# Kernel tuning notes

Hardware: AMD Instinct MI355X
Metric: run time of the kernel (lower is better)

## Reference

```python
import jax, jax.numpy as jnp
import numpy as np

N_FP = 235336   # n_fingerprint
N_WORD = 7844   # n_word
D = 10          # embed / hidden dim (hard-coded in module)
K = 23          # conv kernel 2*11+1
PAD = 11
N_ATOMS = 4096
L_WORDS = 65536


def setup_inputs() -> dict:
    key = jax.random.key(0)
    ks = jax.random.split(key, 16)
    s = 0.1  # weight init scale
    return {
        "fingerprints": jax.random.randint(ks[0], (N_ATOMS,), 0, N_FP),
        # scale adjacency so x + A@hs stays O(1) over 3 layers
        "adjacency": jax.random.uniform(ks[1], (N_ATOMS, N_ATOMS), dtype=jnp.float32) * (1.0 / N_ATOMS),
        "words": jax.random.randint(ks[2], (L_WORDS,), 0, N_WORD),
        "embed_fp": jax.random.normal(ks[3], (N_FP, D), dtype=jnp.float32) * s,
        "embed_word": jax.random.normal(ks[4], (N_WORD, D), dtype=jnp.float32) * s,
        "W_gnn_w": jax.random.normal(ks[5], (3, D, D), dtype=jnp.float32) * s,
        "W_gnn_b": jax.random.normal(ks[6], (3, D), dtype=jnp.float32) * s,
        "W_cnn_w": jax.random.normal(ks[7], (3, 1, 1, K, K), dtype=jnp.float32) * (s / K),
        "W_cnn_b": jax.random.normal(ks[8], (3,), dtype=jnp.float32) * s,
        "W_att_w": jax.random.normal(ks[9], (D, D), dtype=jnp.float32) * s,
        "W_att_b": jax.random.normal(ks[10], (D,), dtype=jnp.float32) * s,
        "W_out_w": jax.random.normal(ks[11], (3, 2 * D, 2 * D), dtype=jnp.float32) * s,
        "W_out_b": jax.random.normal(ks[12], (3, 2 * D), dtype=jnp.float32) * s,
        "W_int_w": jax.random.normal(ks[13], (2, 2 * D), dtype=jnp.float32) * s,
        "W_int_b": jax.random.normal(ks[14], (2,), dtype=jnp.float32) * s,
    }


def reference(fingerprints, adjacency, words, embed_fp, embed_word,
              W_gnn_w, W_gnn_b, W_cnn_w, W_cnn_b, W_att_w, W_att_b,
              W_out_w, W_out_b, W_int_w, W_int_b):
    # ---- Compound vector with GNN ----
    xs = embed_fp[fingerprints]                       # [N, D]
    for i in range(3):                                # fixed 3 layers
        hs = jax.nn.relu(xs @ W_gnn_w[i].T + W_gnn_b[i])
        xs = xs + adjacency @ hs                      # dense message passing
    compound = jnp.mean(xs, axis=0, keepdims=True)    # [1, D]

    # ---- Protein vector with attention-CNN ----
    ws = embed_word[words]                            # [L, D]
    t = ws[None, None]                                # [1,1,L,D] NCHW
    for i in range(3):
        t = jax.nn.relu(
            jax.lax.conv_general_dilated(t, W_cnn_w[i], (1, 1),
                                          [(PAD, PAD), (PAD, PAD)])
            + W_cnn_b[i])
    xs_p = t[0, 0]                                    # [L, D]

    h = jax.nn.relu(compound @ W_att_w.T + W_att_b)   # [1, D]
    hs_p = jax.nn.relu(xs_p @ W_att_w.T + W_att_b)    # [L, D]
    weights = jnp.tanh(h @ hs_p.T)                    # [1, L]
    ys = weights.T * hs_p                             # [L, D]
    protein = jnp.mean(ys, axis=0, keepdims=True)     # [1, D]

    # ---- Fusion MLP ----
    cat = jnp.concatenate([compound, protein], axis=1)  # [1, 2D]
    for j in range(3):
        cat = jax.nn.relu(cat @ W_out_w[j].T + W_out_b[j])
    return cat @ W_int_w.T + W_int_b                  # [1, 2]
```

## Files before the change

### kernel.cpp

```cpp
#include <hip/hip_runtime.h>
#include <math.h>

#define N_ATOMS 4096
#define L_WORDS 65536
#define DD 10
#define HALO 11

#define CONV_BLOCKS 256
#define CONV_BLOCK 256
#define RPW 8
#define RPB 32
#define QCOLS 1024
#define TOTAL_BLOCKS 768
#define ATT_BLOCKS 64

__global__ __launch_bounds__(128) void gnn_embed(
    const int* __restrict__ fp, const float* __restrict__ embed_fp,
    const float* __restrict__ Wg, const float* __restrict__ bg,
    float* __restrict__ xs, float* __restrict__ hs)
{
    const int n = blockIdx.x * 128 + threadIdx.x;
    float x[DD];
    const float* e = embed_fp + (size_t)fp[n] * DD;
    #pragma unroll
    for (int d = 0; d < DD; ++d) x[d] = e[d];
    #pragma unroll
    for (int d = 0; d < DD; ++d) xs[d * N_ATOMS + n] = x[d];
    #pragma unroll
    for (int d = 0; d < DD; ++d) {
        float v = bg[d];
        #pragma unroll
        for (int k = 0; k < DD; ++k) v += Wg[d * DD + k] * x[k];
        hs[d * N_ATOMS + n] = fmaxf(v, 0.f);
    }
}

__device__ __forceinline__ void conv_stage(
    float* sh, const int tid, const int bx,
    const float* __restrict__ tin, const int* __restrict__ words,
    const float* __restrict__ embed_word, const float* __restrict__ w,
    const float* __restrict__ bptr, float* __restrict__ tout,
    const float* __restrict__ Wa, const float* __restrict__ ba,
    float* __restrict__ hpb)
{
    const int l0 = bx * CONV_BLOCK;
    for (int idx = tid; idx < (CONV_BLOCK + 2 * HALO) * DD; idx += CONV_BLOCK) {
        int rr = idx / DD, d = idx - rr * DD;
        int gr = l0 - HALO + rr;
        float v = 0.f;
        if (gr >= 0 && gr < L_WORDS) {
            if (tin) v = tin[(size_t)gr * DD + d];
            else     v = embed_word[(size_t)words[gr] * DD + d];
        }
        sh[rr * 11 + d] = v;
    }
    __syncthreads();

    const float bias = *bptr;
    float acc[DD];
    #pragma unroll
    for (int d = 0; d < DD; ++d) acc[d] = bias;
    for (int i = 0; i < 23; ++i) {
        float row[DD];
        const float* sr = &sh[(tid + i) * 11];
        #pragma unroll
        for (int c = 0; c < DD; ++c) row[c] = sr[c];
        #pragma unroll
        for (int d = 0; d < DD; ++d) {
            #pragma unroll
            for (int c = 0; c < DD; ++c)
                acc[d] += row[c] * w[i * 23 + (c - d + 11)];
        }
    }
    const int l = l0 + tid;
    if (tout) {
        #pragma unroll
        for (int d = 0; d < DD; ++d)
            tout[(size_t)l * DD + d] = fmaxf(acc[d], 0.f);
    }
    if (hpb) {
        float xsp[DD];
        #pragma unroll
        for (int d = 0; d < DD; ++d) xsp[d] = fmaxf(acc[d], 0.f);
        #pragma unroll
        for (int d = 0; d < DD; ++d) {
            float v = ba[d];
            #pragma unroll
            for (int k = 0; k < DD; ++k) v += Wa[d * DD + k] * xsp[k];
            hpb[(size_t)l * DD + d] = fmaxf(v, 0.f);
        }
    }
}

__device__ __forceinline__ void gnn_stage(
    float* sh, const int tid, const int b,
    const float* __restrict__ hs_in,
    const float* __restrict__ xs_in, const float* __restrict__ part_in,
    const float* __restrict__ Wg, const float* __restrict__ bg,
    float* __restrict__ xs_out,
    const float* __restrict__ A, float* __restrict__ part_out)
{
    const int wave = tid >> 6, lane = tid & 63;
    const int q = b & 3, rg = b >> 2;
    const int qbase = q * QCOLS;

    if (hs_in) {
        const float4* h4 = (const float4*)hs_in;
        float4* shw = (float4*)sh;
        #pragma unroll
        for (int d = 0; d < DD; ++d)
            shw[d * 256 + tid] = h4[d * (N_ATOMS / 4) + q * 256 + tid];
    } else {
        for (int j = 0; j < 4; ++j) {
            const int lc = j * 256 + tid;
            const int n = qbase + lc;
            float x[DD];
            #pragma unroll
            for (int d = 0; d < DD; ++d) {
                float v = xs_in[d * N_ATOMS + n];
                #pragma unroll
                for (int qq = 0; qq < 4; ++qq)
                    v += part_in[((size_t)qq * DD + d) * N_ATOMS + n];
                x[d] = v;
            }
            if (rg == 0) {
                #pragma unroll
                for (int d = 0; d < DD; ++d) xs_out[d * N_ATOMS + n] = x[d];
            }
            #pragma unroll
            for (int d = 0; d < DD; ++d) {
                float v = bg[d];
                #pragma unroll
                for (int k = 0; k < DD; ++k) v += Wg[d * DD + k] * x[k];
                sh[d * QCOLS + lc] = fmaxf(v, 0.f);
            }
        }
    }
    __syncthreads();

    const int r0 = rg * RPB + wave * RPW;
    const float4* A4 = (const float4*)(A + (size_t)r0 * N_ATOMS) + q * (QCOLS / 4);
    const float4* sh4 = (const float4*)sh;

    float acc[RPW][DD];
    #pragma unroll
    for (int r = 0; r < RPW; ++r)
        #pragma unroll
        for (int d = 0; d < DD; ++d) acc[r][d] = 0.f;

    #pragma unroll 1
    for (int it = 0; it < 4; ++it) {
        const int cb = it * 64 + lane;
        float4 a[RPW];
        #pragma unroll
        for (int r = 0; r < RPW; ++r) a[r] = A4[r * (N_ATOMS / 4) + cb];
        #pragma unroll
        for (int d = 0; d < DD; ++d) {
            float4 h = sh4[d * 256 + cb];
            #pragma unroll
            for (int r = 0; r < RPW; ++r) {
                acc[r][d] += a[r].x * h.x;
                acc[r][d] += a[r].y * h.y;
                acc[r][d] += a[r].z * h.z;
                acc[r][d] += a[r].w * h.w;
            }
        }
    }

    #pragma unroll
    for (int m = 1; m <= 4; m <<= 1) {
        #pragma unroll
        for (int r = 0; r < RPW; ++r)
            #pragma unroll
            for (int d = 0; d < DD; ++d)
                acc[r][d] += __shfl_xor(acc[r][d], m, 64);
    }
    __syncthreads();

    if ((lane & 7) == 0) {
        const int g = lane >> 3;
        float* dst = &sh[(wave * 8 + g) * 80];
        #pragma unroll
        for (int r = 0; r < RPW; ++r)
            #pragma unroll
            for (int d = 0; d < DD; ++d) dst[r * DD + d] = acc[r][d];
    }
    __syncthreads();

    float* pdst = part_out + (size_t)q * DD * N_ATOMS + (size_t)rg * RPB;
    for (int o = tid; o < RPB * DD; o += 256) {
        const int d = o >> 5, rr = o & 31;
        const int w8 = rr >> 3, r = rr & 7;
        float v = 0.f;
        #pragma unroll
        for (int g = 0; g < 8; ++g) v += sh[(w8 * 8 + g) * 80 + r * DD + d];
        pdst[d * N_ATOMS + rr] = v;
    }
}

__global__ __launch_bounds__(256, 3) void fused_layer(
    const float* __restrict__ A, const float* __restrict__ hs_in,
    const float* __restrict__ xs_in, const float* __restrict__ part_in,
    const float* __restrict__ Wg, const float* __restrict__ bg,
    float* __restrict__ xs_out, float* __restrict__ part_out,
    const float* __restrict__ tin, const int* __restrict__ words,
    const float* __restrict__ emb_w, const float* __restrict__ wc,
    const float* __restrict__ bc, float* __restrict__ tout,
    const float* __restrict__ Wa, const float* __restrict__ ba,
    float* __restrict__ hpb)
{
    __shared__ float sh[DD * QCOLS];
    const int tid = threadIdx.x;
    if (blockIdx.x < CONV_BLOCKS)
        conv_stage(sh, tid, blockIdx.x, tin, words, emb_w, wc, bc, tout,
                   Wa, ba, hpb);
    else
        gnn_stage(sh, tid, blockIdx.x - CONV_BLOCKS, hs_in,
                  xs_in, part_in, Wg, bg, xs_out, A, part_out);
}

__global__ __launch_bounds__(1024) void attn_final(
    const float* __restrict__ xs2, const float* __restrict__ part2,
    const float* __restrict__ hpb,
    const float* __restrict__ Wa, const float* __restrict__ ba,
    const float* __restrict__ Wo, const float* __restrict__ bo,
    const float* __restrict__ Wi, const float* __restrict__ bi,
    float* att_part, unsigned int* ticket, float* __restrict__ out)
{
    __shared__ float red[16][DD];
    __shared__ float shc[DD];
    __shared__ float cat[20];
    __shared__ int islast;
    const int tid = threadIdx.x, wave = tid >> 6, lane = tid & 63;

    float c[DD];
    #pragma unroll
    for (int d = 0; d < DD; ++d) c[d] = 0.f;
    #pragma unroll
    for (int s = 0; s < 4; ++s) {
        const int n = s * 1024 + tid;
        #pragma unroll
        for (int d = 0; d < DD; ++d) {
            float v = xs2[d * N_ATOMS + n];
            #pragma unroll
            for (int qq = 0; qq < 4; ++qq)
                v += part2[((size_t)qq * DD + d) * N_ATOMS + n];
            c[d] += v;
        }
    }
    #pragma unroll
    for (int m = 32; m >= 1; m >>= 1) {
        #pragma unroll
        for (int d = 0; d < DD; ++d) c[d] += __shfl_xor(c[d], m, 64);
    }
    if (lane == 0) {
        #pragma unroll
        for (int d = 0; d < DD; ++d) red[wave][d] = c[d];
    }
    __syncthreads();
    if (tid < DD) {
        float v = 0.f;
        #pragma unroll
        for (int w = 0; w < 16; ++w) v += red[w][tid];
        shc[tid] = v * (1.f / N_ATOMS);
    }
    __syncthreads();

    float h[DD];
    #pragma unroll
    for (int d = 0; d < DD; ++d) {
        float v = ba[d];
        #pragma unroll
        for (int k = 0; k < DD; ++k) v += Wa[d * DD + k] * shc[k];
        h[d] = fmaxf(v, 0.f);
    }
    const int w_ = blockIdx.x * 1024 + tid;
    float hp[DD], dotv = 0.f;
    #pragma unroll
    for (int d = 0; d < DD; ++d) {
        hp[d] = hpb[(size_t)w_ * DD + d];
        dotv += h[d] * hp[d];
    }
    const float wgt = tanhf(dotv);
    float y[DD];
    #pragma unroll
    for (int d = 0; d < DD; ++d) y[d] = wgt * hp[d];
    #pragma unroll
    for (int m = 32; m >= 1; m >>= 1) {
        #pragma unroll
        for (int d = 0; d < DD; ++d) y[d] += __shfl_xor(y[d], m, 64);
    }
    __syncthreads();
    if (lane == 0) {
        #pragma unroll
        for (int d = 0; d < DD; ++d) red[wave][d] = y[d];
    }
    __syncthreads();
    if (tid < DD) {
        float v = 0.f;
        #pragma unroll
        for (int w = 0; w < 16; ++w) v += red[w][tid];
        __hip_atomic_store(att_part + blockIdx.x * DD + tid, v,
                           __ATOMIC_RELAXED, __HIP_MEMORY_SCOPE_AGENT);
    }
    __syncthreads();

    if (tid == 0) {
        unsigned prev = __hip_atomic_fetch_add(ticket, 1u, __ATOMIC_RELAXED,
                                               __HIP_MEMORY_SCOPE_AGENT);
        islast = (prev == ATT_BLOCKS - 1);
    }
    __syncthreads();
    if (!islast) return;
    asm volatile("" ::: "memory");

    float a[DD];
    #pragma unroll
    for (int d = 0; d < DD; ++d) a[d] = 0.f;
    if (tid < ATT_BLOCKS) {
        #pragma unroll
        for (int d = 0; d < DD; ++d)
            a[d] = __hip_atomic_load(att_part + tid * DD + d,
                                     __ATOMIC_RELAXED, __HIP_MEMORY_SCOPE_AGENT);
    }
    if (wave == 0) {
        #pragma unroll
        for (int m = 32; m >= 1; m >>= 1) {
            #pragma unroll
            for (int d = 0; d < DD; ++d) a[d] += __shfl_xor(a[d], m, 64);
        }
    }
    if (tid == 0) {
        #pragma unroll
        for (int d = 0; d < DD; ++d) cat[DD + d] = a[d] * (1.f / L_WORDS);
    }
    if (tid < DD) cat[tid] = shc[tid];
    __syncthreads();
    for (int j = 0; j < 3; ++j) {
        float v = 0.f;
        if (tid < 20) {
            v = bo[j * 20 + tid];
            for (int k = 0; k < 20; ++k) v += Wo[j * 400 + tid * 20 + k] * cat[k];
        }
        __syncthreads();
        if (tid < 20) cat[tid] = fmaxf(v, 0.f);
        __syncthreads();
    }
    if (tid < 2) {
        float v = bi[tid];
        for (int k = 0; k < 20; ++k) v += Wi[tid * 20 + k] * cat[k];
        out[tid] = v;
    }
}

extern "C" void kernel_launch(void* const* d_in, const int* in_sizes, int n_in,
                              void* d_out, int out_size, void* d_ws, size_t ws_size,
                              hipStream_t stream)
{
    const int*   fp     = (const int*)d_in[0];
    const float* A      = (const float*)d_in[1];
    const int*   words  = (const int*)d_in[2];
    const float* emb_fp = (const float*)d_in[3];
    const float* emb_w  = (const float*)d_in[4];
    const float* Wg     = (const float*)d_in[5];
    const float* bg     = (const float*)d_in[6];
    const float* Wc     = (const float*)d_in[7];
    const float* bc     = (const float*)d_in[8];
    const float* Wa     = (const float*)d_in[9];
    const float* ba     = (const float*)d_in[10];
    const float* Wo     = (const float*)d_in[11];
    const float* bo     = (const float*)d_in[12];
    const float* Wi     = (const float*)d_in[13];
    const float* bi     = (const float*)d_in[14];
    float* out = (float*)d_out;
    float* ws  = (float*)d_ws;

    float* xs0   = ws;
    float* xs1   = ws + 40960;
    float* xs2   = ws + 81920;
    float* hs0   = ws + 122880;
    float* part0 = ws + 163840;
    float* part1 = ws + 327680;
    float* part2 = ws + 491520;
    float* ta    = ws + 655360;
    float* tb    = ws + 1310720;
    float* hpb   = ta;
    float* att_part = ws + 1966080;
    unsigned int* ticket = (unsigned int*)(ws + 1966720);

    hipMemsetAsync(ticket, 0, sizeof(unsigned int), stream);

    gnn_embed<<<N_ATOMS / 128, 128, 0, stream>>>(fp, emb_fp, Wg, bg, xs0, hs0);

    fused_layer<<<TOTAL_BLOCKS, 256, 0, stream>>>(
        A, hs0, nullptr, nullptr, Wg, bg, nullptr, part0,
        nullptr, words, emb_w, Wc, bc, ta, nullptr, nullptr, nullptr);

    fused_layer<<<TOTAL_BLOCKS, 256, 0, stream>>>(
        A, nullptr, xs0, part0, Wg + 100, bg + 10, xs1, part1,
        ta, words, emb_w, Wc + 529, bc + 1, tb, nullptr, nullptr, nullptr);

    fused_layer<<<TOTAL_BLOCKS, 256, 0, stream>>>(
        A, nullptr, xs1, part1, Wg + 200, bg + 20, xs2, part2,
        tb, words, emb_w, Wc + 1058, bc + 2, nullptr, Wa, ba, hpb);

    attn_final<<<ATT_BLOCKS, 1024, 0, stream>>>(
        xs2, part2, hpb, Wa, ba, Wo, bo, Wi, bi, att_part, ticket, out);
}
```

Baseline: 203.9 us.

## Prefetch adjacency tiles ahead of LDS staging and double-buffer A loads

The first adjacency float4 tile is loaded into registers before the hs staging into shared memory, so global latency overlaps the staging work. The main loop prefetches the next tile while computing on the current one. The reduction scratch moves to a separate shared-memory region, which removes one __syncthreads. Shared memory grows and register pressure roughly doubles for the A tiles, which could lower occupancy under the launch bound of 3 blocks.

```diff
diff --git a/kernel.cpp b/kernel.cpp
--- a/kernel.cpp
+++ b/kernel.cpp
@@ -13,6 +13,7 @@
 #define QCOLS 1024
 #define TOTAL_BLOCKS 768
 #define ATT_BLOCKS 64
+#define STASH 10240
 
 __global__ __launch_bounds__(128) void gnn_embed(
     const int* __restrict__ fp, const float* __restrict__ embed_fp,
@@ -103,6 +104,12 @@
     const int wave = tid >> 6, lane = tid & 63;
     const int q = b & 3, rg = b >> 2;
     const int qbase = q * QCOLS;
+
+    const int r0 = rg * RPB + wave * RPW;
+    const float4* A4 = (const float4*)(A + (size_t)r0 * N_ATOMS) + q * (QCOLS / 4);
+    float4 a_cur[RPW];
+    #pragma unroll
+    for (int r = 0; r < RPW; ++r) a_cur[r] = A4[r * (N_ATOMS / 4) + lane];
 
     if (hs_in) {
         const float4* h4 = (const float4*)hs_in;
@@ -138,8 +145,6 @@
     }
     __syncthreads();
 
-    const int r0 = rg * RPB + wave * RPW;
-    const float4* A4 = (const float4*)(A + (size_t)r0 * N_ATOMS) + q * (QCOLS / 4);
     const float4* sh4 = (const float4*)sh;
 
     float acc[RPW][DD];
@@ -151,19 +156,26 @@
     #pragma unroll 1
     for (int it = 0; it < 4; ++it) {
         const int cb = it * 64 + lane;
-        float4 a[RPW];
-        #pragma unroll
-        for (int r = 0; r < RPW; ++r) a[r] = A4[r * (N_ATOMS / 4) + cb];
+        float4 a_nxt[RPW];
+        if (it < 3) {
+            #pragma unroll
+            for (int r = 0; r < RPW; ++r)
+                a_nxt[r] = A4[r * (N_ATOMS / 4) + cb + 64];
+        }
         #pragma unroll
         for (int d = 0; d < DD; ++d) {
             float4 h = sh4[d * 256 + cb];
             #pragma unroll
             for (int r = 0; r < RPW; ++r) {
-                acc[r][d] += a[r].x * h.x;
-                acc[r][d] += a[r].y * h.y;
-                acc[r][d] += a[r].z * h.z;
-                acc[r][d] += a[r].w * h.w;
+                acc[r][d] += a_cur[r].x * h.x;
+                acc[r][d] += a_cur[r].y * h.y;
+                acc[r][d] += a_cur[r].z * h.z;
+                acc[r][d] += a_cur[r].w * h.w;
             }
+        }
+        if (it < 3) {
+            #pragma unroll
+            for (int r = 0; r < RPW; ++r) a_cur[r] = a_nxt[r];
         }
     }
 
@@ -175,11 +187,10 @@
             for (int d = 0; d < DD; ++d)
                 acc[r][d] += __shfl_xor(acc[r][d], m, 64);
     }
-    __syncthreads();
 
     if ((lane & 7) == 0) {
         const int g = lane >> 3;
-        float* dst = &sh[(wave * 8 + g) * 80];
+        float* dst = &sh[STASH + (wave * 8 + g) * 80];
         #pragma unroll
         for (int r = 0; r < RPW; ++r)
             #pragma unroll
@@ -193,7 +204,8 @@
         const int w8 = rr >> 3, r = rr & 7;
         float v = 0.f;
         #pragma unroll
-        for (int g = 0; g < 8; ++g) v += sh[(w8 * 8 + g) * 80 + r * DD + d];
+        for (int g = 0; g < 8; ++g)
+            v += sh[STASH + (w8 * 8 + g) * 80 + r * DD + d];
         pdst[d * N_ATOMS + rr] = v;
     }
 }
@@ -209,7 +221,7 @@
     const float* __restrict__ Wa, const float* __restrict__ ba,
     float* __restrict__ hpb)
 {
-    __shared__ float sh[DD * QCOLS];
+    __shared__ float sh[STASH + RPB * 80];
     const int tid = threadIdx.x;
     if (blockIdx.x < CONV_BLOCKS)
         conv_stage(sh, tid, blockIdx.x, tin, words, emb_w, wc, bc, tout,
```

After: 390.2 us. 1.91x slower.

## Split GNN layer prep into separate kernel and read hs directly from global

Applied to the files above, without the earlier changes.

Moves the per-layer xs update and hs computation out of each GNN block into a small gnn_prep kernel, so 512 blocks no longer each recompute 1024 atoms' worth of prep. The matmul loop now reads hs straight from global/L2 instead of staging it in shared memory, which shrinks the shared array and may allow more resident blocks. The cost is two extra kernel launches and extra global traffic for the hs reads in the inner loop.

```diff
diff --git a/kernel.cpp b/kernel.cpp
--- a/kernel.cpp
+++ b/kernel.cpp
@@ -13,6 +13,7 @@
 #define QCOLS 1024
 #define TOTAL_BLOCKS 768
 #define ATT_BLOCKS 64
+#define SH_FLOATS 2926
 
 __global__ __launch_bounds__(128) void gnn_embed(
     const int* __restrict__ fp, const float* __restrict__ embed_fp,
@@ -26,6 +27,31 @@
     for (int d = 0; d < DD; ++d) x[d] = e[d];
     #pragma unroll
     for (int d = 0; d < DD; ++d) xs[d * N_ATOMS + n] = x[d];
+    #pragma unroll
+    for (int d = 0; d < DD; ++d) {
+        float v = bg[d];
+        #pragma unroll
+        for (int k = 0; k < DD; ++k) v += Wg[d * DD + k] * x[k];
+        hs[d * N_ATOMS + n] = fmaxf(v, 0.f);
+    }
+}
+
+__global__ __launch_bounds__(128) void gnn_prep(
+    const float* __restrict__ xs_in, const float* __restrict__ part,
+    const float* __restrict__ Wg, const float* __restrict__ bg,
+    float* __restrict__ xs_out, float* __restrict__ hs)
+{
+    const int n = blockIdx.x * 128 + threadIdx.x;
+    float x[DD];
+    #pragma unroll
+    for (int d = 0; d < DD; ++d) {
+        float v = xs_in[d * N_ATOMS + n];
+        #pragma unroll
+        for (int q = 0; q < 4; ++q)
+            v += part[((size_t)q * DD + d) * N_ATOMS + n];
+        x[d] = v;
+        xs_out[d * N_ATOMS + n] = v;
+    }
     #pragma unroll
     for (int d = 0; d < DD; ++d) {
         float v = bg[d];
@@ -94,53 +120,15 @@
 
 __device__ __forceinline__ void gnn_stage(
     float* sh, const int tid, const int b,
-    const float* __restrict__ hs_in,
-    const float* __restrict__ xs_in, const float* __restrict__ part_in,
-    const float* __restrict__ Wg, const float* __restrict__ bg,
-    float* __restrict__ xs_out,
+    const float* __restrict__ hs,
     const float* __restrict__ A, float* __restrict__ part_out)
 {
     const int wave = tid >> 6, lane = tid & 63;
     const int q = b & 3, rg = b >> 2;
-    const int qbase = q * QCOLS;
-
-    if (hs_in) {
-        const float4* h4 = (const float4*)hs_in;
-        float4* shw = (float4*)sh;
-        #pragma unroll
-        for (int d = 0; d < DD; ++d)
-            shw[d * 256 + tid] = h4[d * (N_ATOMS / 4) + q * 256 + tid];
-    } else {
-        for (int j = 0; j < 4; ++j) {
-            const int lc = j * 256 + tid;
-            const int n = qbase + lc;
-            float x[DD];
-            #pragma unroll
-            for (int d = 0; d < DD; ++d) {
-                float v = xs_in[d * N_ATOMS + n];
-                #pragma unroll
-                for (int qq = 0; qq < 4; ++qq)
-                    v += part_in[((size_t)qq * DD + d) * N_ATOMS + n];
-                x[d] = v;
-            }
-            if (rg == 0) {
-                #pragma unroll
-                for (int d = 0; d < DD; ++d) xs_out[d * N_ATOMS + n] = x[d];
-            }
-            #pragma unroll
-            for (int d = 0; d < DD; ++d) {
-                float v = bg[d];
-                #pragma unroll
-                for (int k = 0; k < DD; ++k) v += Wg[d * DD + k] * x[k];
-                sh[d * QCOLS + lc] = fmaxf(v, 0.f);
-            }
-        }
-    }
-    __syncthreads();
 
     const int r0 = rg * RPB + wave * RPW;
     const float4* A4 = (const float4*)(A + (size_t)r0 * N_ATOMS) + q * (QCOLS / 4);
-    const float4* sh4 = (const float4*)sh;
+    const float4* h4 = (const float4*)hs + q * (QCOLS / 4);
 
     float acc[RPW][DD];
     #pragma unroll
@@ -156,7 +144,7 @@
         for (int r = 0; r < RPW; ++r) a[r] = A4[r * (N_ATOMS / 4) + cb];
         #pragma unroll
         for (int d = 0; d < DD; ++d) {
-            float4 h = sh4[d * 256 + cb];
+            float4 h = h4[d * (N_ATOMS / 4) + cb];
             #pragma unroll
             for (int r = 0; r < RPW; ++r) {
                 acc[r][d] += a[r].x * h.x;
@@ -175,7 +163,6 @@
             for (int d = 0; d < DD; ++d)
                 acc[r][d] += __shfl_xor(acc[r][d], m, 64);
     }
-    __syncthreads();
 
     if ((lane & 7) == 0) {
         const int g = lane >> 3;
@@ -199,24 +186,21 @@
 }
 
 __global__ __launch_bounds__(256, 3) void fused_layer(
-    const float* __restrict__ A, const float* __restrict__ hs_in,
-    const float* __restrict__ xs_in, const float* __restrict__ part_in,
-    const float* __restrict__ Wg, const float* __restrict__ bg,
-    float* __restrict__ xs_out, float* __restrict__ part_out,
+    const float* __restrict__ A, const float* __restrict__ hs,
+    float* __restrict__ part_out,
     const float* __restrict__ tin, const int* __restrict__ words,
     const float* __restrict__ emb_w, const float* __restrict__ wc,
     const float* __restrict__ bc, float* __restrict__ tout,
     const float* __restrict__ Wa, const float* __restrict__ ba,
     float* __restrict__ hpb)
 {
-    __shared__ float sh[DD * QCOLS];
+    __shared__ float sh[SH_FLOATS];
     const int tid = threadIdx.x;
     if (blockIdx.x < CONV_BLOCKS)
         conv_stage(sh, tid, blockIdx.x, tin, words, emb_w, wc, bc, tout,
                    Wa, ba, hpb);
     else
-        gnn_stage(sh, tid, blockIdx.x - CONV_BLOCKS, hs_in,
-                  xs_in, part_in, Wg, bg, xs_out, A, part_out);
+        gnn_stage(sh, tid, blockIdx.x - CONV_BLOCKS, hs, A, part_out);
 }
 
 __global__ __launch_bounds__(1024) void attn_final(
@@ -379,29 +363,37 @@
     float* xs1   = ws + 40960;
     float* xs2   = ws + 81920;
     float* hs0   = ws + 122880;
-    float* part0 = ws + 163840;
-    float* part1 = ws + 327680;
-    float* part2 = ws + 491520;
-    float* ta    = ws + 655360;
-    float* tb    = ws + 1310720;
+    float* hs1   = ws + 163840;
+    float* hs2   = ws + 204800;
+    float* part0 = ws + 245760;
+    float* part1 = ws + 409600;
+    float* part2 = ws + 573440;
+    float* ta    = ws + 737280;
+    float* tb    = ws + 1392640;
     float* hpb   = ta;
-    float* att_part = ws + 1966080;
-    unsigned int* ticket = (unsigned int*)(ws + 1966720);
+    float* att_part = ws + 2048000;
+    unsigned int* ticket = (unsigned int*)(ws + 2048640);
 
     hipMemsetAsync(ticket, 0, sizeof(unsigned int), stream);
 
     gnn_embed<<<N_ATOMS / 128, 128, 0, stream>>>(fp, emb_fp, Wg, bg, xs0, hs0);
 
     fused_layer<<<TOTAL_BLOCKS, 256, 0, stream>>>(
-        A, hs0, nullptr, nullptr, Wg, bg, nullptr, part0,
+        A, hs0, part0,
         nullptr, words, emb_w, Wc, bc, ta, nullptr, nullptr, nullptr);
 
+    gnn_prep<<<N_ATOMS / 128, 128, 0, stream>>>(
+        xs0, part0, Wg + 100, bg + 10, xs1, hs1);
+
     fused_layer<<<TOTAL_BLOCKS, 256, 0, stream>>>(
-        A, nullptr, xs0, part0, Wg + 100, bg + 10, xs1, part1,
+        A, hs1, part1,
         ta, words, emb_w, Wc + 529, bc + 1, tb, nullptr, nullptr, nullptr);
 
+    gnn_prep<<<N_ATOMS / 128, 128, 0, stream>>>(
+        xs1, part1, Wg + 200, bg + 20, xs2, hs2);
+
     fused_layer<<<TOTAL_BLOCKS, 256, 0, stream>>>(
-        A, nullptr, xs1, part1, Wg + 200, bg + 20, xs2, part2,
+        A, hs2, part2,
         tb, words, emb_w, Wc + 1058, bc + 2, nullptr, Wa, ba, hpb);
 
     attn_final<<<ATT_BLOCKS, 1024, 0, stream>>>(
```

New measurement: 206.3 us. No clear change (+1.2%).
